# Performance work log

Measured on AMD Instinct MI355X. Metric: run time of the kernel, lower is better.

The kernel has to match this reference:

```python
import jax, jax.numpy as jnp
import numpy as np
import math

B, S, E, H = 2, 2048, 1024, 8
Dh = E // H  # 128


def setup_inputs() -> dict:
    key = jax.random.key(0)
    ks = jax.random.split(key, 9)
    g = lambda k, shp: jax.random.normal(k, shp, jnp.float32) * 0.02
    return {
        "inputs": jax.random.normal(ks[0], (B, S, E), jnp.float32),
        "ln_gamma": jnp.ones((E,), jnp.float32),
        "ln_beta": jnp.zeros((E,), jnp.float32),
        "Wq": g(ks[1], (Dh, Dh)), "bq": jnp.zeros((Dh,), jnp.float32),
        "Wk": g(ks[2], (Dh, Dh)), "bk": jnp.zeros((Dh,), jnp.float32),
        "Wv": g(ks[3], (Dh, Dh)), "bv": jnp.zeros((Dh,), jnp.float32),
        "Wp": g(ks[4], (Dh, Dh)),  # pos_proj has no bias
        "u_bias": g(ks[5], (H, Dh)),
        "v_bias": g(ks[6], (H, Dh)),
        "Wo": g(ks[7], (E, E)), "bo": jnp.zeros((E,), jnp.float32),
    }


def _pos_encoding(s, e):
    # sinusoidal PE, interleaved sin/cos as in the torch module
    pos = jnp.arange(s, dtype=jnp.float32)[:, None]
    div = jnp.exp(jnp.arange(0, e, 2, dtype=jnp.float32) * (-math.log(10000.0) / e))
    pe = jnp.zeros((s, e), jnp.float32)
    pe = pe.at[:, 0::2].set(jnp.sin(pos * div))
    pe = pe.at[:, 1::2].set(jnp.cos(pos * div))
    return pe


def _rel_shift(ps):
    # Transformer-XL relative shift: pad a zero column, reshape, drop first row
    b, h, s1, s2 = ps.shape
    padded = jnp.pad(ps, ((0, 0), (0, 0), (0, 0), (1, 0)))
    return padded.reshape(b, h, s2 + 1, s1)[:, :, 1:, :].reshape(b, h, s1, s2)


def _forward(inputs, ln_gamma, ln_beta, Wq, bq, Wk, bk, Wv, bv, Wp, u_bias, v_bias, Wo, bo):
    b, s, e = inputs.shape
    # LayerNorm (biased variance, eps=1e-5 like nn.LayerNorm)
    mu = inputs.mean(-1, keepdims=True)
    var = inputs.var(-1, keepdims=True)
    xn = (inputs - mu) / jnp.sqrt(var + 1e-5) * ln_gamma + ln_beta

    xh = xn.reshape(b, s, H, Dh)              # split heads before per-head Dh x Dh projections
    q = xh @ Wq + bq                           # (b, s, H, Dh)
    k = xh @ Wk + bk
    v = xh @ Wv + bv

    pe = _pos_encoding(s, e).reshape(s, H, Dh)  # same for every batch element
    p = pe @ Wp                                 # (s, H, Dh)

    content = jnp.einsum('bqhd,bkhd->bhqk', q + u_bias, k)
    pos_score = jnp.einsum('bqhd,khd->bhqk', q + v_bias, p)
    pos_score = _rel_shift(pos_score)
    score = (content + pos_score) / jnp.sqrt(jnp.float32(e))  # note: scales by sqrt(embed_dim), faithful to source

    attn = jax.nn.softmax(score, axis=-1)
    ctx = jnp.einsum('bhqk,bkhd->bqhd', attn, v).reshape(b, s, e)
    # dropout is identity at inference
    return ctx @ Wo + bo


def reference(inputs, ln_gamma, ln_beta, Wq, bq, Wk, bk, Wv, bv, Wp, u_bias, v_bias, Wo, bo):
    return _forward(inputs, ln_gamma, ln_beta, Wq, bq, Wk, bk, Wv, bv, Wp, u_bias, v_bias, Wo, bo)
```

## Files before the change

### kernel.cpp

```cpp
#include <hip/hip_runtime.h>
#include <hip/hip_bf16.h>

#define SDIM 2048
#define EDIM 1024

typedef __attribute__((ext_vector_type(8))) short bf16x8;
typedef __attribute__((ext_vector_type(4))) short bf16x4;
typedef __attribute__((ext_vector_type(4))) float f32x4;
typedef __hip_bfloat16 bf16;

#define MFMA(a, b, c) __builtin_amdgcn_mfma_f32_16x16x32_bf16((a), (b), (c), 0, 0, 0)

#define GLDS16(g, l)                                                      \
  __builtin_amdgcn_global_load_lds(                                       \
      (const __attribute__((address_space(1))) unsigned int*)(g),         \
      (__attribute__((address_space(3))) unsigned int*)(l), 16, 0, 0)

__device__ __forceinline__ bf16x8 ld8(const bf16* p) {
  return *(const bf16x8*)p;
}
__device__ __forceinline__ float b2f(short s) {
  union { float f; unsigned u; } v; v.u = ((unsigned)(unsigned short)s) << 16; return v.f;
}
__device__ __forceinline__ float fexp2(float x) {
  float r;
  asm("v_exp_f32 %0, %1" : "=v"(r) : "v"(x));
  return r;
}

__device__ __forceinline__ void wcast_body(const float* __restrict__ w, bf16* __restrict__ wt,
                                           int blk, int R, int C) {
  __shared__ float tile[32][33];
  int cb = C >> 5;
  int br = blk / cb, bc = blk % cb;
  int r0 = br << 5, c0 = bc << 5;
  int tr = threadIdx.x >> 5, tc = threadIdx.x & 31;
#pragma unroll
  for (int i = 0; i < 32; i += 8)
    tile[tr + i][tc] = w[(size_t)(r0 + tr + i) * C + c0 + tc];
  __syncthreads();
#pragma unroll
  for (int i = 0; i < 32; i += 8)
    wt[(size_t)(c0 + tr + i) * R + r0 + tc] = __float2bfloat16(tile[tc][tr + i]);
}

__global__ __launch_bounds__(256) void wcast_all(const float* __restrict__ wo, const float* __restrict__ w0,
                                                 const float* __restrict__ w1, const float* __restrict__ w2,
                                                 const float* __restrict__ w3, bf16* __restrict__ oo,
                                                 bf16* __restrict__ o0, bf16* __restrict__ o1,
                                                 bf16* __restrict__ o2, bf16* __restrict__ o3) {
  int blk = blockIdx.x;
  if (blk < 1024) {
    wcast_body(wo, oo, blk, 1024, 1024);
  } else {
    int which = (blk - 1024) >> 4;
    const float* w = which == 0 ? w0 : which == 1 ? w1 : which == 2 ? w2 : w3;
    bf16* o = which == 0 ? o0 : which == 1 ? o1 : which == 2 ? o2 : o3;
    wcast_body(w, o, (blk - 1024) & 15, 128, 128);
  }
}

__global__ __launch_bounds__(256) void ln_kernel(const float* __restrict__ x, const float* __restrict__ g,
                                                 const float* __restrict__ be, bf16* __restrict__ xn) {
  int tok = blockIdx.x;
  const float4 v = ((const float4*)(x + (size_t)tok * EDIM))[threadIdx.x];
  float s = v.x + v.y + v.z + v.w;
  float s2 = v.x * v.x + v.y * v.y + v.z * v.z + v.w * v.w;
#pragma unroll
  for (int o = 1; o < 64; o <<= 1) { s += __shfl_xor(s, o); s2 += __shfl_xor(s2, o); }
  __shared__ float ls[8];
  if ((threadIdx.x & 63) == 0) { ls[threadIdx.x >> 6] = s; ls[4 + (threadIdx.x >> 6)] = s2; }
  __syncthreads();
  s = ls[0] + ls[1] + ls[2] + ls[3];
  s2 = ls[4] + ls[5] + ls[6] + ls[7];
  float mu = s * (1.0f / EDIM);
  float rstd = rsqrtf(s2 * (1.0f / EDIM) - mu * mu + 1e-5f);
  int c = threadIdx.x * 4;
  const float4 gv = ((const float4*)g)[threadIdx.x];
  const float4 bv = ((const float4*)be)[threadIdx.x];
  bf16* o = xn + (size_t)tok * EDIM + c;
  o[0] = __float2bfloat16((v.x - mu) * rstd * gv.x + bv.x);
  o[1] = __float2bfloat16((v.y - mu) * rstd * gv.y + bv.y);
  o[2] = __float2bfloat16((v.z - mu) * rstd * gv.z + bv.z);
  o[3] = __float2bfloat16((v.w - mu) * rstd * gv.w + bv.w);
}

__global__ __launch_bounds__(256) void pe_kernel(bf16* __restrict__ pe) {
  int s = blockIdx.x;
  for (int i = threadIdx.x; i < EDIM / 2; i += 256) {
    float div = __expf((float)(2 * i) * (-9.210340371976184f / (float)EDIM));
    float a = (float)s * div;
    float sv, cv;
    sincosf(a, &sv, &cv);
    pe[(size_t)s * EDIM + 2 * i] = __float2bfloat16(sv);
    pe[(size_t)s * EDIM + 2 * i + 1] = __float2bfloat16(cv);
  }
}

#define QSCALE 0.045084219879837156f
template <int MODE>
__device__ __forceinline__ void proj_body(const bf16* __restrict__ A, const bf16* __restrict__ WT,
                                          const float* __restrict__ bias, const float* __restrict__ ubias,
                                          const float* __restrict__ vbias, bf16* __restrict__ out0,
                                          bf16* __restrict__ out1, int blk, bf16* tl) {
  const int row0 = blk * 128;
  const int lane = threadIdx.x & 63, wid = threadIdx.x >> 6;
  const int wr = (wid >> 1) * 64, wc = (wid & 1) * 64;
  const int lg = lane >> 4, lr = lane & 15;
  f32x4 acc[4][4] = {};
#pragma unroll
  for (int kf = 0; kf < 4; ++kf) {
    const int k0 = kf * 32 + lg * 8;
    bf16x8 a[4], b[4];
#pragma unroll
    for (int m = 0; m < 4; ++m) a[m] = ld8(A + (size_t)(row0 + wr + m * 16 + lr) * 128 + k0);
#pragma unroll
    for (int n = 0; n < 4; ++n) b[n] = ld8(WT + (size_t)(wc + n * 16 + lr) * 128 + k0);
#pragma unroll
    for (int m = 0; m < 4; ++m)
#pragma unroll
      for (int n = 0; n < 4; ++n) acc[m][n] = MFMA(a[m], b[n], acc[m][n]);
  }
  if constexpr (MODE == 2) {
#pragma unroll
    for (int m = 0; m < 4; ++m)
#pragma unroll
      for (int n = 0; n < 4; ++n) {
        int col = wc + n * 16 + lr;
#pragma unroll
        for (int r = 0; r < 4; ++r) {
          int lrow = wr + m * 16 + lg * 4 + r;
          tl[col * 132 + lrow] = __float2bfloat16(acc[m][n][r] + bias[col]);
        }
      }
    __syncthreads();
    int tok0 = row0 >> 3;
    int b = tok0 >> 11, s0 = tok0 & 2047;
#pragma unroll
    for (int i = 0; i < 4; ++i) {
      int pair = threadIdx.x + 256 * i;
      int h = pair >> 7, d = pair & 127;
      bf16 tmp[16];
#pragma unroll
      for (int j = 0; j < 16; ++j) tmp[j] = tl[d * 132 + j * 8 + h];
      size_t o = ((size_t)((b * 8 + h) * 128 + d)) * SDIM + s0;
      *(bf16x8*)(out0 + o) = *(bf16x8*)(&tmp[0]);
      *(bf16x8*)(out0 + o + 8) = *(bf16x8*)(&tmp[8]);
    }
  } else {
#pragma unroll
    for (int m = 0; m < 4; ++m)
#pragma unroll
      for (int n = 0; n < 4; ++n) {
        int col = wc + n * 16 + lr;
#pragma unroll
        for (int r = 0; r < 4; ++r) {
          int row = row0 + wr + m * 16 + lg * 4 + r;
          float val = acc[m][n][r];
          if constexpr (MODE == 0) {
            int h = row & 7, tok = row >> 3;
            int b = tok >> 11, s = tok & 2047;
            size_t o = ((size_t)((b * 8 + h) * SDIM + s)) * 128 + col;
            val += bias[col];
            out0[o] = __float2bfloat16((val + ubias[h * 128 + col]) * QSCALE);
            out1[o] = __float2bfloat16((val + vbias[h * 128 + col]) * QSCALE);
          } else if constexpr (MODE == 1) {
            int h = row & 7, tok = row >> 3;
            int b = tok >> 11, s = tok & 2047;
            out0[((size_t)((b * 8 + h) * SDIM + s)) * 128 + col] = __float2bfloat16(val + bias[col]);
          } else {
            int h = row & 7, s = row >> 3;
            out0[((size_t)(h * SDIM + s)) * 128 + col] = __float2bfloat16(val);
          }
        }
      }
  }
}

__global__ __launch_bounds__(256) void proj_all(const bf16* __restrict__ xn, const bf16* __restrict__ peb,
                                                const bf16* __restrict__ wqt, const bf16* __restrict__ wkt,
                                                const bf16* __restrict__ wvt, const bf16* __restrict__ wpt,
                                                const float* __restrict__ bq, const float* __restrict__ bk,
                                                const float* __restrict__ bv, const float* __restrict__ ub,
                                                const float* __restrict__ vbias, bf16* __restrict__ qub,
                                                bf16* __restrict__ qvb, bf16* __restrict__ kbb,
                                                bf16* __restrict__ vtb, bf16* __restrict__ pb) {
  __shared__ bf16 tl[128 * 132];
  int blk = blockIdx.x;
  if (blk < 256) proj_body<0>(xn, wqt, bq, ub, vbias, qub, qvb, blk, tl);
  else if (blk < 512) proj_body<1>(xn, wkt, bk, nullptr, nullptr, kbb, nullptr, blk - 256, tl);
  else if (blk < 768) proj_body<2>(xn, wvt, bv, nullptr, nullptr, vtb, nullptr, blk - 512, tl);
  else proj_body<3>(peb, wpt, nullptr, nullptr, nullptr, pb, nullptr, blk - 768, tl);
}

__global__ __launch_bounds__(256) void ps_kernel(const bf16* __restrict__ qv, const bf16* __restrict__ p,
                                                 bf16* __restrict__ ps) {
  const int bh = blockIdx.x & 15;
  const int t = blockIdx.x >> 4;
  const int q0 = (t >> 4) * 128, j0 = (t & 15) * 128;
  const int h = bh & 7;
  const bf16* Aq = qv + (size_t)bh * SDIM * 128;
  const bf16* Ph = p + (size_t)h * SDIM * 128;
  const int lane = threadIdx.x & 63, wid = threadIdx.x >> 6;
  const int wr = (wid >> 1) * 64, wc = (wid & 1) * 64;
  const int lg = lane >> 4, lr = lane & 15;
  f32x4 acc[4][4] = {};
#pragma unroll
  for (int kf = 0; kf < 4; ++kf) {
    const int k0 = kf * 32 + lg * 8;
    bf16x8 a[4], b[4];
#pragma unroll
    for (int m = 0; m < 4; ++m) a[m] = ld8(Aq + (size_t)(q0 + wr + m * 16 + lr) * 128 + k0);
#pragma unroll
    for (int n = 0; n < 4; ++n) b[n] = ld8(Ph + (size_t)(j0 + wc + n * 16 + lr) * 128 + k0);
#pragma unroll
    for (int m = 0; m < 4; ++m)
#pragma unroll
      for (int n = 0; n < 4; ++n) acc[m][n] = MFMA(a[m], b[n], acc[m][n]);
  }
  __shared__ bf16 tl[128 * 136];
#pragma unroll
  for (int m = 0; m < 4; ++m)
#pragma unroll
    for (int n = 0; n < 4; ++n) {
      int jl = wc + n * 16 + lr;
#pragma unroll
      for (int r = 0; r < 4; ++r) {
        int ql = wr + m * 16 + lg * 4 + r;
        tl[ql * 136 + jl] = __float2bfloat16(acc[m][n][r]);
      }
    }
  __syncthreads();
  bf16* po = ps + (size_t)bh * SDIM * SDIM + (size_t)q0 * SDIM + j0;
#pragma unroll
  for (int i = 0; i < 8; ++i) {
    int id = threadIdx.x + 256 * i;
    int row = id >> 4, seg = id & 15;
    bf16x8 v = *(const bf16x8*)(tl + row * 136 + seg * 8);
    *(bf16x8*)(po + (size_t)row * SDIM + seg * 8) = v;
  }
}

#define PSLOAD(KT, WLO, WHI)                                              \
  {                                                                       \
    _Pragma("unroll")                                                     \
    for (int nf = 0; nf < 4; ++nf) {                                      \
      const int K0 = (KT) + nf * 16 + lg * 4;                             \
      const bool a_ = (K0 + 3 <= Q);                                      \
      const bf16* wp = a_ ? (pA + K0 - padA) : (pB + K0 - padB);          \
      WLO[nf] = *(const unsigned long long*)wp;                           \
      WHI[nf] = *(const unsigned long long*)(wp + 4);                     \
    }                                                                     \
  }

#define STAGE(KT, BUF)                                                    \
  {                                                                       \
    _Pragma("unroll")                                                     \
    for (int i = 0; i < 2; ++i) {                                         \
      int rb = wid * 8 + i * 4;                                           \
      int row = rb + krow_l;                                              \
      GLDS16(Kp + (size_t)((KT) + row) * 128 + ((kc16 ^ (row & 7)) << 3), \
             &kl[BUF][rb * 128]);                                         \
    }                                                                     \
    _Pragma("unroll")                                                     \
    for (int i = 0; i < 2; ++i) {                                         \
      int rb = wid * 16 + i * 8;                                          \
      int d = rb + vrow_l;                                                \
      GLDS16(Vp + (size_t)d * SDIM + (KT) + ((vc8 ^ (d & 7)) << 3),       \
             &vl[BUF][rb * 64]);                                          \
    }                                                                     \
  }

#define TILE(KT, BUF, WLO, WHI, WLO2, WHI2, PREF)                         \
  {                                                                       \
    if (PREF) { STAGE((KT) + 64, BUF ^ 1); }                              \
    const bf16* klc = &kl[BUF][0];                                        \
    const bf16* vlc = &vl[BUF][0];                                        \
    f32x4 sc[4] = {};                                                     \
    __builtin_amdgcn_s_setprio(1);                                        \
    _Pragma("unroll")                                                     \
    for (int nf = 0; nf < 4; ++nf) {                                      \
      const int krow = nf * 16 + lr;                                      \
      const bf16* kr = klc + krow * 128;                                  \
      const int sw = (krow & 7) << 3;                                     \
      _Pragma("unroll")                                                   \
      for (int kf = 0; kf < 4; ++kf) {                                    \
        bf16x8 kfrag = *(const bf16x8*)(kr + (((kf * 4 + lg) << 3) ^ sw));\
        sc[nf] = MFMA(kfrag, qfr[kf], sc[nf]);                            \
      }                                                                   \
    }                                                                     \
    __builtin_amdgcn_s_setprio(0);                                        \
    bf16x4 pscur[4];                                                      \
    _Pragma("unroll")                                                     \
    for (int nf = 0; nf < 4; ++nf) {                                      \
      const int K0 = (KT) + nf * 16 + lg * 4;                             \
      const bool a_ = (K0 + 3 <= Q);                                      \
      const bool bp = (K0 >= Q + 2);                                      \
      const int sh = (a_ ? padA : padB) << 4;                             \
      unsigned long long w =                                              \
          sh ? ((WLO[nf] >> sh) | (WHI[nf] << (64 - sh))) : WLO[nf];      \
      union { unsigned long long u; bf16x4 v; } cv;                       \
      cv.u = w;                                                           \
      bf16x4 pv = cv.v;                                                   \
      if (!a_ && !bp) {                                                   \
        _Pragma("unroll")                                                 \
        for (int r = 0; r < 4; ++r) {                                     \
          const int K = K0 + r;                                           \
          if (K <= Q) pv[r] = ((const short*)pA)[K];                      \
          else if (K == Q + 1) pv[r] = (short)0;                          \
        }                                                                 \
      }                                                                   \
      pscur[nf] = pv;                                                     \
    }                                                                     \
    if (PREF) { PSLOAD((KT) + 64, WLO2, WHI2); }                          \
    _Pragma("unroll")                                                     \
    for (int nf = 0; nf < 4; ++nf) {                                      \
      float e0 = fexp2(sc[nf][0] + b2f(pscur[nf][0]));                    \
      float e1 = fexp2(sc[nf][1] + b2f(pscur[nf][1]));                    \
      float e2 = fexp2(sc[nf][2] + b2f(pscur[nf][2]));                    \
      float e3 = fexp2(sc[nf][3] + b2f(pscur[nf][3]));                    \
      rsum += (e0 + e1) + (e2 + e3);                                      \
      bf16 tmp[4] = {__float2bfloat16(e0), __float2bfloat16(e1),          \
                     __float2bfloat16(e2), __float2bfloat16(e3)};         \
      *(bf16x4*)(plw + lr * 72 + nf * 16 + lg * 4) = *(bf16x4*)tmp;       \
    }                                                                     \
    bf16x8 pa[2];                                                         \
    _Pragma("unroll")                                                     \
    for (int k2 = 0; k2 < 2; ++k2)                                        \
      pa[k2] = *(const bf16x8*)(plw + lr * 72 + k2 * 32 + lg * 8);        \
    __builtin_amdgcn_s_setprio(1);                                        \
    _Pragma("unroll")                                                     \
    for (int nf = 0; nf < 8; ++nf) {                                      \
      const int d = nf * 16 + lr;                                         \
      const bf16* vr = vlc + d * 64;                                      \
      const int swd = (d & 7) << 3;                                       \
      _Pragma("unroll")                                                   \
      for (int k2 = 0; k2 < 2; ++k2) {                                    \
        bf16x8 vb = *(const bf16x8*)(vr + (((k2 * 4 + lg) << 3) ^ swd));  \
        cacc[nf] = MFMA(pa[k2], vb, cacc[nf]);                            \
      }                                                                   \
    }                                                                     \
    __builtin_amdgcn_s_setprio(0);                                        \
    asm volatile("s_waitcnt vmcnt(8)" ::: "memory");                      \
    __builtin_amdgcn_s_barrier();                                         \
  }

__global__ __launch_bounds__(512) void attn_kernel(const bf16* __restrict__ qu, const bf16* __restrict__ kb,
                                                   const bf16* __restrict__ vt, const bf16* __restrict__ ps,
                                                   bf16* __restrict__ ctx) {
  const int bh = blockIdx.x & 15, qblk = blockIdx.x >> 4;
  const int b = bh >> 3, h = bh & 7;
  const int lane = threadIdx.x & 63, wid = threadIdx.x >> 6;
  const int lg = lane >> 4, lr = lane & 15;
  const int q0 = qblk * 128 + wid * 16;
  const bf16* Kp = kb + (size_t)bh * SDIM * 128;
  const bf16* Vp = vt + (size_t)bh * 128 * SDIM;

  const bf16* psbh = ps + (size_t)bh * SDIM * SDIM;
  const int Q = q0 + lr;
  const bf16* pA = psbh + (size_t)(Q + 1) * (SDIM - 1);
  const bf16* pB = psbh + (size_t)(Q + 1) * SDIM - Q - 2;
  const int padA = (int)(((unsigned)(Q + 1) * (SDIM - 1)) & 3);
  const int padB = (int)(((unsigned)(Q + 1) * SDIM - Q - 2) & 3);

  __shared__ bf16 kl[2][64 * 128];
  __shared__ bf16 vl[2][128 * 64];
  __shared__ bf16 pl[8][16 * 72];
  bf16* plw = &pl[wid][0];

  const int krow_l = lane >> 4, kc16 = lane & 15;
  const int vrow_l = lane >> 3, vc8 = lane & 7;

  bf16x8 qfr[4];
#pragma unroll
  for (int kf = 0; kf < 4; ++kf)
    qfr[kf] = ld8(qu + (size_t)bh * SDIM * 128 + (size_t)(q0 + lr) * 128 + kf * 32 + lg * 8);

  f32x4 cacc[8] = {};
  float rsum = 0.f;

  unsigned long long wloA[4], whiA[4], wloB[4], whiB[4];

  STAGE(0, 0);
  PSLOAD(0, wloA, whiA);
  asm volatile("s_waitcnt vmcnt(8)" ::: "memory");
  __builtin_amdgcn_s_barrier();

  for (int t2 = 0; t2 < 32; t2 += 2) {
    const int kt = t2 * 64;
    TILE(kt, 0, wloA, whiA, wloB, whiB, true);
    TILE(kt + 64, 1, wloB, whiB, wloA, whiA, (t2 + 2 < 32));
  }

  rsum += __shfl_xor(rsum, 16);
  rsum += __shfl_xor(rsum, 32);
  float inv[4];
#pragma unroll
  for (int r = 0; r < 4; ++r) inv[r] = 1.0f / __shfl(rsum, lg * 4 + r);
#pragma unroll
  for (int nf = 0; nf < 8; ++nf) {
#pragma unroll
    for (int r = 0; r < 4; ++r) {
      int q = q0 + lg * 4 + r;
      int d = nf * 16 + lr;
      ctx[((size_t)(b * SDIM + q) * 8 + h) * 128 + d] = __float2bfloat16(cacc[nf][r] * inv[r]);
    }
  }
}

__global__ __launch_bounds__(256) void out_gemm(const bf16* __restrict__ A, const bf16* __restrict__ WT,
                                                const float* __restrict__ bo, float* __restrict__ out) {
  const int bm = blockIdx.x >> 3, bn = blockIdx.x & 7;
  const int lane = threadIdx.x & 63, wid = threadIdx.x >> 6;
  const int wr = (wid >> 1) * 64, wc = (wid & 1) * 64;
  const int lg = lane >> 4, lr = lane & 15;
  const int row0 = bm * 128, col0 = bn * 128;
  f32x4 acc[4][4] = {};
  for (int kf = 0; kf < 32; ++kf) {
    const int k0 = kf * 32 + lg * 8;
    bf16x8 a[4], b[4];
#pragma unroll
    for (int m = 0; m < 4; ++m) a[m] = ld8(A + (size_t)(row0 + wr + m * 16 + lr) * 1024 + k0);
#pragma unroll
    for (int n = 0; n < 4; ++n) b[n] = ld8(WT + (size_t)(col0 + wc + n * 16 + lr) * 1024 + k0);
#pragma unroll
    for (int m = 0; m < 4; ++m)
#pragma unroll
      for (int n = 0; n < 4; ++n) acc[m][n] = MFMA(a[m], b[n], acc[m][n]);
  }
#pragma unroll
  for (int m = 0; m < 4; ++m)
#pragma unroll
    for (int n = 0; n < 4; ++n) {
      int col = col0 + wc + n * 16 + lr;
#pragma unroll
      for (int r = 0; r < 4; ++r) {
        int row = row0 + wr + m * 16 + lg * 4 + r;
        out[(size_t)row * 1024 + col] = acc[m][n][r] + bo[col];
      }
    }
}

extern "C" void kernel_launch(void* const* d_in, const int* in_sizes, int n_in,
                              void* d_out, int out_size, void* d_ws, size_t ws_size,
                              hipStream_t stream) {
  (void)in_sizes; (void)n_in; (void)out_size;
  const float* x = (const float*)d_in[0];
  const float* gam = (const float*)d_in[1];
  const float* bet = (const float*)d_in[2];
  const float* Wq = (const float*)d_in[3];
  const float* bq = (const float*)d_in[4];
  const float* Wk = (const float*)d_in[5];
  const float* bk = (const float*)d_in[6];
  const float* Wv = (const float*)d_in[7];
  const float* bv = (const float*)d_in[8];
  const float* Wp = (const float*)d_in[9];
  const float* ub = (const float*)d_in[10];
  const float* vbias = (const float*)d_in[11];
  const float* Wo = (const float*)d_in[12];
  const float* bo = (const float*)d_in[13];
  float* out = (float*)d_out;

  char* w = (char*)d_ws;
  size_t off = 0;
  auto take = [&](size_t n) { void* p = w + off; off += (n + 255) & ~(size_t)255; return p; };
  bf16* xn = (bf16*)take((size_t)4096 * 1024 * 2);
  bf16* peb = (bf16*)take((size_t)2048 * 1024 * 2);
  bf16* wqt = (bf16*)take(128 * 128 * 2);
  bf16* wkt = (bf16*)take(128 * 128 * 2);
  bf16* wvt = (bf16*)take(128 * 128 * 2);
  bf16* wpt = (bf16*)take(128 * 128 * 2);
  bf16* wot = (bf16*)take((size_t)1024 * 1024 * 2);
  bf16* qub = (bf16*)take((size_t)16 * 2048 * 128 * 2);
  bf16* qvb = (bf16*)take((size_t)16 * 2048 * 128 * 2);
  bf16* kbb = (bf16*)take((size_t)16 * 2048 * 128 * 2);
  bf16* vtb = (bf16*)take((size_t)16 * 2048 * 128 * 2);
  bf16* pb = (bf16*)take((size_t)8 * 2048 * 128 * 2);
  bf16* ctx = (bf16*)take((size_t)4096 * 1024 * 2);
  bf16* psb = (bf16*)take((size_t)16 * 2048 * 2048 * 2 + 4096);
  if (off > ws_size) return;

  wcast_all<<<1088, 256, 0, stream>>>(Wo, Wq, Wk, Wv, Wp, wot, wqt, wkt, wvt, wpt);
  ln_kernel<<<4096, 256, 0, stream>>>(x, gam, bet, xn);
  pe_kernel<<<2048, 256, 0, stream>>>(peb);
  proj_all<<<896, 256, 0, stream>>>(xn, peb, wqt, wkt, wvt, wpt, bq, bk, bv, ub, vbias,
                                    qub, qvb, kbb, vtb, pb);
  ps_kernel<<<4096, 256, 0, stream>>>(qvb, pb, psb);
  attn_kernel<<<256, 512, 0, stream>>>(qub, kbb, vtb, psb, ctx);
  out_gemm<<<256, 256, 0, stream>>>(ctx, wot, bo, out);
}
```

Before: 209.0 us.

## Rewrite attention kernel with 32x32x16 MFMA and register-resident probabilities

Switches the attention kernel from 16x16x32 MFMA tiles to 32x32x16 tiles, giving each wave 32 query rows. Probabilities are packed to bf16 in registers and rearranged with cross-lane shuffles, so they no longer go through LDS before the PV product. The launch changes from 256 blocks of 512 threads to 512 blocks of 128 threads, and each wave stages more K/V tiles. This adds register pressure and lowers waves per block, which could hurt latency hiding.

Result: slower. 233.2 us (+11.6%).

```diff
diff --git a/kernel.cpp b/kernel.cpp
--- a/kernel.cpp
+++ b/kernel.cpp
@@ -7,9 +7,11 @@
 typedef __attribute__((ext_vector_type(8))) short bf16x8;
 typedef __attribute__((ext_vector_type(4))) short bf16x4;
 typedef __attribute__((ext_vector_type(4))) float f32x4;
+typedef __attribute__((ext_vector_type(16))) float f32x16;
 typedef __hip_bfloat16 bf16;
 
 #define MFMA(a, b, c) __builtin_amdgcn_mfma_f32_16x16x32_bf16((a), (b), (c), 0, 0, 0)
+#define MFMA32(a, b, c) __builtin_amdgcn_mfma_f32_32x32x16_bf16((a), (b), (c), 0, 0, 0)
 
 #define GLDS16(g, l)                                                      \
   __builtin_amdgcn_global_load_lds(                                       \
@@ -25,6 +27,11 @@
 __device__ __forceinline__ float fexp2(float x) {
   float r;
   asm("v_exp_f32 %0, %1" : "=v"(r) : "v"(x));
+  return r;
+}
+__device__ __forceinline__ unsigned cvtpk(float lo, float hi) {
+  unsigned r;
+  asm("v_cvt_pk_bf16_f32 %0, %1, %2" : "=v"(r) : "v"(lo), "v"(hi));
   return r;
 }
 
@@ -244,61 +251,46 @@
 #define PSLOAD(KT, WLO, WHI)                                              \
   {                                                                       \
     _Pragma("unroll")                                                     \
-    for (int nf = 0; nf < 4; ++nf) {                                      \
-      const int K0 = (KT) + nf * 16 + lg * 4;                             \
-      const bool a_ = (K0 + 3 <= Q);                                      \
-      const bf16* wp = a_ ? (pA + K0 - padA) : (pB + K0 - padB);          \
-      WLO[nf] = *(const unsigned long long*)wp;                           \
-      WHI[nf] = *(const unsigned long long*)(wp + 4);                     \
-    }                                                                     \
+    for (int tt = 0; tt < 2; ++tt)                                        \
+      _Pragma("unroll")                                                   \
+      for (int R = 0; R < 4; ++R) {                                       \
+        const int K0 = (KT) + tt * 32 + R * 8 + hl * 4;                   \
+        const bool a_ = (K0 + 3 <= Q);                                    \
+        const bf16* wp = a_ ? (pA + K0 - padA) : (pB + K0 - padB);        \
+        WLO[tt * 4 + R] = *(const unsigned long long*)wp;                 \
+        WHI[tt * 4 + R] = *(const unsigned long long*)(wp + 4);           \
+      }                                                                   \
   }
 
 #define STAGE(KT, BUF)                                                    \
   {                                                                       \
     _Pragma("unroll")                                                     \
-    for (int i = 0; i < 2; ++i) {                                         \
-      int rb = wid * 8 + i * 4;                                           \
+    for (int i = 0; i < 8; ++i) {                                         \
+      int rb = wid * 32 + i * 4;                                          \
       int row = rb + krow_l;                                              \
       GLDS16(Kp + (size_t)((KT) + row) * 128 + ((kc16 ^ (row & 7)) << 3), \
              &kl[BUF][rb * 128]);                                         \
     }                                                                     \
     _Pragma("unroll")                                                     \
-    for (int i = 0; i < 2; ++i) {                                         \
-      int rb = wid * 16 + i * 8;                                          \
+    for (int i = 0; i < 8; ++i) {                                         \
+      int rb = wid * 64 + i * 8;                                          \
       int d = rb + vrow_l;                                                \
       GLDS16(Vp + (size_t)d * SDIM + (KT) + ((vc8 ^ (d & 7)) << 3),       \
              &vl[BUF][rb * 64]);                                          \
     }                                                                     \
   }
 
-#define TILE(KT, BUF, WLO, WHI, WLO2, WHI2, PREF)                         \
+#define SMHALF(TT, SC, KT, WLO, WHI)                                      \
   {                                                                       \
-    if (PREF) { STAGE((KT) + 64, BUF ^ 1); }                              \
-    const bf16* klc = &kl[BUF][0];                                        \
-    const bf16* vlc = &vl[BUF][0];                                        \
-    f32x4 sc[4] = {};                                                     \
-    __builtin_amdgcn_s_setprio(1);                                        \
     _Pragma("unroll")                                                     \
-    for (int nf = 0; nf < 4; ++nf) {                                      \
-      const int krow = nf * 16 + lr;                                      \
-      const bf16* kr = klc + krow * 128;                                  \
-      const int sw = (krow & 7) << 3;                                     \
-      _Pragma("unroll")                                                   \
-      for (int kf = 0; kf < 4; ++kf) {                                    \
-        bf16x8 kfrag = *(const bf16x8*)(kr + (((kf * 4 + lg) << 3) ^ sw));\
-        sc[nf] = MFMA(kfrag, qfr[kf], sc[nf]);                            \
-      }                                                                   \
-    }                                                                     \
-    __builtin_amdgcn_s_setprio(0);                                        \
-    bf16x4 pscur[4];                                                      \
-    _Pragma("unroll")                                                     \
-    for (int nf = 0; nf < 4; ++nf) {                                      \
-      const int K0 = (KT) + nf * 16 + lg * 4;                             \
+    for (int R = 0; R < 4; ++R) {                                         \
+      const int idx = TT * 4 + R;                                         \
+      const int K0 = (KT) + TT * 32 + R * 8 + hl * 4;                     \
       const bool a_ = (K0 + 3 <= Q);                                      \
       const bool bp = (K0 >= Q + 2);                                      \
       const int sh = (a_ ? padA : padB) << 4;                             \
       unsigned long long w =                                              \
-          sh ? ((WLO[nf] >> sh) | (WHI[nf] << (64 - sh))) : WLO[nf];      \
+          sh ? ((WLO[idx] >> sh) | (WHI[idx] << (64 - sh))) : WLO[idx];   \
       union { unsigned long long u; bf16x4 v; } cv;                       \
       cv.u = w;                                                           \
       bf16x4 pv = cv.v;                                                   \
@@ -310,54 +302,79 @@
           else if (K == Q + 1) pv[r] = (short)0;                          \
         }                                                                 \
       }                                                                   \
-      pscur[nf] = pv;                                                     \
+      float e0 = fexp2(SC[4 * R + 0] + b2f(pv[0]));                       \
+      float e1 = fexp2(SC[4 * R + 1] + b2f(pv[1]));                       \
+      float e2 = fexp2(SC[4 * R + 2] + b2f(pv[2]));                       \
+      float e3 = fexp2(SC[4 * R + 3] + b2f(pv[3]));                       \
+      rsum += (e0 + e1) + (e2 + e3);                                      \
+      xk[idx * 2 + 0] = cvtpk(e0, e1);                                    \
+      xk[idx * 2 + 1] = cvtpk(e2, e3);                                    \
     }                                                                     \
-    if (PREF) { PSLOAD((KT) + 64, WLO2, WHI2); }                          \
-    _Pragma("unroll")                                                     \
-    for (int nf = 0; nf < 4; ++nf) {                                      \
-      float e0 = fexp2(sc[nf][0] + b2f(pscur[nf][0]));                    \
-      float e1 = fexp2(sc[nf][1] + b2f(pscur[nf][1]));                    \
-      float e2 = fexp2(sc[nf][2] + b2f(pscur[nf][2]));                    \
-      float e3 = fexp2(sc[nf][3] + b2f(pscur[nf][3]));                    \
-      rsum += (e0 + e1) + (e2 + e3);                                      \
-      bf16 tmp[4] = {__float2bfloat16(e0), __float2bfloat16(e1),          \
-                     __float2bfloat16(e2), __float2bfloat16(e3)};         \
-      *(bf16x4*)(plw + lr * 72 + nf * 16 + lg * 4) = *(bf16x4*)tmp;       \
-    }                                                                     \
-    bf16x8 pa[2];                                                         \
-    _Pragma("unroll")                                                     \
-    for (int k2 = 0; k2 < 2; ++k2)                                        \
-      pa[k2] = *(const bf16x8*)(plw + lr * 72 + k2 * 32 + lg * 8);        \
+  }
+
+#define TILE(KT, BUF, WLO, WHI, WLO2, WHI2, PREF)                         \
+  {                                                                       \
+    if (PREF) { STAGE((KT) + 64, BUF ^ 1); }                              \
+    asm volatile("" ::: "memory");                                        \
+    const bf16* klc = &kl[BUF][0];                                        \
+    const bf16* vlc = &vl[BUF][0];                                        \
+    f32x16 sc0 = {};                                                      \
+    f32x16 sc1 = {};                                                      \
     __builtin_amdgcn_s_setprio(1);                                        \
     _Pragma("unroll")                                                     \
-    for (int nf = 0; nf < 8; ++nf) {                                      \
-      const int d = nf * 16 + lr;                                         \
-      const bf16* vr = vlc + d * 64;                                      \
-      const int swd = (d & 7) << 3;                                       \
+    for (int kf = 0; kf < 8; ++kf) {                                      \
+      bf16x8 k0f = *(const bf16x8*)(klc + m * 128 + (((2 * kf + hl) ^ (m & 7)) << 3)); \
+      bf16x8 k1f = *(const bf16x8*)(klc + (32 + m) * 128 + (((2 * kf + hl) ^ (m & 7)) << 3)); \
+      sc0 = MFMA32(k0f, qfr[kf], sc0);                                    \
+      sc1 = MFMA32(k1f, qfr[kf], sc1);                                    \
+    }                                                                     \
+    __builtin_amdgcn_s_setprio(0);                                        \
+    unsigned xk[16];                                                      \
+    SMHALF(0, sc0, KT, WLO, WHI);                                         \
+    SMHALF(1, sc1, KT, WLO, WHI);                                         \
+    if (PREF) { PSLOAD((KT) + 64, WLO2, WHI2); }                          \
+    asm volatile("" ::: "memory");                                        \
+    __builtin_amdgcn_s_setprio(1);                                        \
+    _Pragma("unroll")                                                     \
+    for (int kk = 0; kk < 4; ++kk) {                                      \
+      const int ia = ((kk >> 1) * 4 + (kk & 1) * 2) * 2;                  \
+      const int ib = ia + 2;                                              \
+      unsigned i0 = xk[ia], i1 = xk[ia + 1];                              \
+      unsigned j0v = xk[ib], j1v = xk[ib + 1];                            \
+      unsigned si0 = (unsigned)__shfl_xor((int)i0, 32);                   \
+      unsigned si1 = (unsigned)__shfl_xor((int)i1, 32);                   \
+      unsigned sj0 = (unsigned)__shfl_xor((int)j0v, 32);                  \
+      unsigned sj1 = (unsigned)__shfl_xor((int)j1v, 32);                  \
+      union { unsigned u[4]; bf16x8 v; } pu;                              \
+      pu.u[0] = hl ? sj0 : i0;                                            \
+      pu.u[1] = hl ? sj1 : i1;                                            \
+      pu.u[2] = hl ? j0v : si0;                                           \
+      pu.u[3] = hl ? j1v : si1;                                           \
       _Pragma("unroll")                                                   \
-      for (int k2 = 0; k2 < 2; ++k2) {                                    \
-        bf16x8 vb = *(const bf16x8*)(vr + (((k2 * 4 + lg) << 3) ^ swd));  \
-        cacc[nf] = MFMA(pa[k2], vb, cacc[nf]);                            \
+      for (int dt = 0; dt < 4; ++dt) {                                    \
+        const int d = dt * 32 + m;                                        \
+        bf16x8 vb = *(const bf16x8*)(vlc + d * 64 + (((2 * kk + hl) ^ (d & 7)) << 3)); \
+        cacc[dt] = MFMA32(pu.v, vb, cacc[dt]);                            \
       }                                                                   \
     }                                                                     \
     __builtin_amdgcn_s_setprio(0);                                        \
-    asm volatile("s_waitcnt vmcnt(8)" ::: "memory");                      \
+    asm volatile("s_waitcnt vmcnt(16)" ::: "memory");                     \
     __builtin_amdgcn_s_barrier();                                         \
   }
 
-__global__ __launch_bounds__(512) void attn_kernel(const bf16* __restrict__ qu, const bf16* __restrict__ kb,
-                                                   const bf16* __restrict__ vt, const bf16* __restrict__ ps,
-                                                   bf16* __restrict__ ctx) {
+__global__ __launch_bounds__(128, 1) void attn_kernel(const bf16* __restrict__ qu, const bf16* __restrict__ kb,
+                                                      const bf16* __restrict__ vt, const bf16* __restrict__ ps,
+                                                      bf16* __restrict__ ctx) {
   const int bh = blockIdx.x & 15, qblk = blockIdx.x >> 4;
-  const int b = bh >> 3, h = bh & 7;
+  const int b = bh >> 3, h_head = bh & 7;
   const int lane = threadIdx.x & 63, wid = threadIdx.x >> 6;
-  const int lg = lane >> 4, lr = lane & 15;
-  const int q0 = qblk * 128 + wid * 16;
+  const int m = lane & 31, hl = lane >> 5;
+  const int q0 = qblk * 64 + wid * 32;
   const bf16* Kp = kb + (size_t)bh * SDIM * 128;
   const bf16* Vp = vt + (size_t)bh * 128 * SDIM;
 
   const bf16* psbh = ps + (size_t)bh * SDIM * SDIM;
-  const int Q = q0 + lr;
+  const int Q = q0 + m;
   const bf16* pA = psbh + (size_t)(Q + 1) * (SDIM - 1);
   const bf16* pB = psbh + (size_t)(Q + 1) * SDIM - Q - 2;
   const int padA = (int)(((unsigned)(Q + 1) * (SDIM - 1)) & 3);
@@ -365,25 +382,24 @@
 
   __shared__ bf16 kl[2][64 * 128];
   __shared__ bf16 vl[2][128 * 64];
-  __shared__ bf16 pl[8][16 * 72];
-  bf16* plw = &pl[wid][0];
 
   const int krow_l = lane >> 4, kc16 = lane & 15;
   const int vrow_l = lane >> 3, vc8 = lane & 7;
 
-  bf16x8 qfr[4];
-#pragma unroll
-  for (int kf = 0; kf < 4; ++kf)
-    qfr[kf] = ld8(qu + (size_t)bh * SDIM * 128 + (size_t)(q0 + lr) * 128 + kf * 32 + lg * 8);
-
-  f32x4 cacc[8] = {};
+  bf16x8 qfr[8];
+#pragma unroll
+  for (int kf = 0; kf < 8; ++kf)
+    qfr[kf] = ld8(qu + ((size_t)bh * SDIM + q0 + m) * 128 + kf * 16 + hl * 8);
+
+  f32x16 cacc[4] = {};
   float rsum = 0.f;
 
-  unsigned long long wloA[4], whiA[4], wloB[4], whiB[4];
+  unsigned long long wloA[8], whiA[8], wloB[8], whiB[8];
 
   STAGE(0, 0);
+  asm volatile("" ::: "memory");
   PSLOAD(0, wloA, whiA);
-  asm volatile("s_waitcnt vmcnt(8)" ::: "memory");
+  asm volatile("s_waitcnt vmcnt(16)" ::: "memory");
   __builtin_amdgcn_s_barrier();
 
   for (int t2 = 0; t2 < 32; t2 += 2) {
@@ -392,20 +408,20 @@
     TILE(kt + 64, 1, wloB, whiB, wloA, whiA, (t2 + 2 < 32));
   }
 
-  rsum += __shfl_xor(rsum, 16);
   rsum += __shfl_xor(rsum, 32);
-  float inv[4];
-#pragma unroll
-  for (int r = 0; r < 4; ++r) inv[r] = 1.0f / __shfl(rsum, lg * 4 + r);
-#pragma unroll
-  for (int nf = 0; nf < 8; ++nf) {
-#pragma unroll
-    for (int r = 0; r < 4; ++r) {
-      int q = q0 + lg * 4 + r;
-      int d = nf * 16 + lr;
-      ctx[((size_t)(b * SDIM + q) * 8 + h) * 128 + d] = __float2bfloat16(cacc[nf][r] * inv[r]);
+  float inv = 1.0f / rsum;
+#pragma unroll
+  for (int R = 0; R < 4; ++R)
+#pragma unroll
+    for (int j = 0; j < 4; ++j) {
+      int qloc = R * 8 + hl * 4 + j;
+      float iv = __shfl(inv, qloc);
+#pragma unroll
+      for (int dt = 0; dt < 4; ++dt) {
+        ctx[((size_t)(b * SDIM + q0 + qloc) * 8 + h_head) * 128 + dt * 32 + m] =
+            __float2bfloat16(cacc[dt][R * 4 + j] * iv);
+      }
     }
-  }
 }
 
 __global__ __launch_bounds__(256) void out_gemm(const bf16* __restrict__ A, const bf16* __restrict__ WT,
@@ -486,6 +502,6 @@
   proj_all<<<896, 256, 0, stream>>>(xn, peb, wqt, wkt, wvt, wpt, bq, bk, bv, ub, vbias,
                                     qub, qvb, kbb, vtb, pb);
   ps_kernel<<<4096, 256, 0, stream>>>(qvb, pb, psb);
-  attn_kernel<<<256, 512, 0, stream>>>(qub, kbb, vtb, psb, ctx);
+  attn_kernel<<<512, 128, 0, stream>>>(qub, kbb, vtb, psb, ctx);
   out_gemm<<<256, 256, 0, stream>>>(ctx, wot, bo, out);
 }
```
